# Kernel tuning notes

Measured on AMD Instinct MI355X. Metric: run time of the kernel, lower is better.

## Reference

```python
import jax, jax.numpy as jnp
import numpy as np
from jax import lax

B, T, L, D, K, VOCAB = 64, 128, 32, 128, 64, 50000


def setup_inputs() -> dict:
    key = jax.random.key(0)
    ks = jax.random.split(key, 8)
    prgrph = jax.random.randint(ks[0], (B, T, L), 0, VOCAB, dtype=jnp.int32)
    prgrph_mask = jax.random.randint(ks[1], (B, T, L), 0, 2, dtype=jnp.int32).astype(bool)
    embedding_matrix = jax.random.normal(ks[2], (VOCAB, D), dtype=jnp.float32)
    positional_mask = jax.random.normal(ks[3], (L, D), dtype=jnp.float32)
    Uw = jax.random.normal(ks[4], (D, D), dtype=jnp.float32) * 0.05
    Vw = jax.random.normal(ks[5], (D, D), dtype=jnp.float32) * 0.05
    Ww = jax.random.normal(ks[6], (D, D), dtype=jnp.float32) * 0.05
    keys = jax.random.normal(ks[7], (B, K, D), dtype=jnp.float32)
    return {"prgrph": prgrph, "prgrph_mask": prgrph_mask,
            "embedding_matrix": embedding_matrix, "positional_mask": positional_mask,
            "Uw": Uw, "Vw": Vw, "Ww": Ww, "keys": keys}


def _entity_scan(enc, sent_mask, keys, Uw, Vw, Ww):
    # enc: [B,T,D] encoded sentences; sent_mask: [B,T] bool; keys: [B,K,D]
    h0 = jnp.zeros_like(keys)  # initial entity hidden state = zeros

    def step(h, xs):
        s, m = xs  # s: [B,D], m: [B]
        # Eq 2: gate = sigmoid(s . h + s . k)  -> [B,K]
        g = jax.nn.sigmoid(jnp.einsum('bkd,bd->bk', h + keys, s))
        # Eq 3: h_tilda = sigmoid(h U + k V + s W)  -> [B,K,D]
        h_tilda = jax.nn.sigmoid(
            jnp.einsum('bkd,de->bke', h, Uw)
            + jnp.einsum('bkd,de->bke', keys, Vw)
            + (s @ Ww)[:, None, :])
        # Eq 4-5: add gated update, L2-normalize over embedding dim
        hn = h + g[..., None] * h_tilda
        hn = hn / jnp.sqrt(jnp.maximum(jnp.sum(hn * hn, axis=-1, keepdims=True), 1e-12))
        # only paragraphs with an active sentence at this step are updated
        h = jnp.where(m[:, None, None], hn, h)
        return h, None

    h_last, _ = lax.scan(step, h0, (jnp.swapaxes(enc, 0, 1), sent_mask.T))
    return h_last


def reference(prgrph, prgrph_mask, embedding_matrix, positional_mask, Uw, Vw, Ww, keys):
    # embed words; padded words contribute zero to the sentence encoding
    emb = embedding_matrix[prgrph] * prgrph_mask[..., None].astype(embedding_matrix.dtype)  # [B,T,L,D]
    # Sent_encoder: weighted bag of words with learned positional mask
    enc = jnp.einsum('btld,ld->btd', emb, positional_mask)  # [B,T,D]
    sent_mask = jnp.any(prgrph_mask, axis=2)  # [B,T]
    return _entity_scan(enc, sent_mask, keys, Uw, Vw, Ww)  # [B,K,D]
```

## Files before the change

### kernel.cpp

```cpp
#include <hip/hip_runtime.h>
#include <hip/hip_bf16.h>
#include <stdint.h>

#define B_ 64
#define T_ 128
#define L_ 32
#define D_ 128
#define K_ 64

#define FLAG_OFF 0
#define SM_OFF   256
#define ENC_OFF  (SM_OFF + B_*T_)
#define SW_OFF   (ENC_OFF + B_*T_*D_)
#define KS_OFF   (SW_OFF + B_*T_*D_)
#define KV_OFF   (KS_OFF + B_*T_*K_)

typedef __attribute__((ext_vector_type(8))) short short8b;
typedef __attribute__((ext_vector_type(4))) float f32x4;

__device__ __forceinline__ float sigmoidf_(float x){ return 1.0f/(1.0f + __expf(-x)); }

__device__ __forceinline__ unsigned short bfb(float x){
  __hip_bfloat16 h = __float2bfloat16(x);
  return __builtin_bit_cast(unsigned short, h);
}
__device__ __forceinline__ float bf2f(unsigned short u){
  return __uint_as_float(((unsigned)u) << 16);
}

__global__ __launch_bounds__(256) void k_detect(const uint8_t* __restrict__ m,
                                                int* __restrict__ flags){
  const unsigned* w = (const unsigned*)m;
  const int base = blockIdx.x * 512;
  unsigned acc = 0;
  acc |= w[base + threadIdx.x]       & 0xFFFFFF00u;
  acc |= w[base + threadIdx.x + 256] & 0xFFFFFF00u;
  int any = __syncthreads_or((int)(acc != 0u));
  if(threadIdx.x == 0) flags[blockIdx.x] = any;
}

__global__ __launch_bounds__(128) void k_enc(const int* __restrict__ prg,
                                             const uint8_t* __restrict__ pm8,
                                             const float* __restrict__ emb,
                                             const float* __restrict__ pos,
                                             const float* __restrict__ Ww,
                                             const float* __restrict__ keys,
                                             float* __restrict__ W){
  const int bt = blockIdx.x;
  const int b  = bt / T_;
  const int d  = threadIdx.x;
  int myf  = ((const int*)W)[FLAG_OFF + (d & 127)];
  int flag = __syncthreads_or(myf);
  __shared__ float keysl[K_*129];
  __shared__ float encl[D_];
  for(int r=0;r<K_;r++) keysl[r*129 + d] = keys[(b*K_ + r)*D_ + d];
  const int* pmi = (const int*)pm8;
  float acc = 0.f; int anym = 0;
  for(int l=0;l<L_;l++){
    int off = bt*L_ + l;
    int m = flag ? (int)pm8[off] : pmi[off];
    if(m){
      anym = 1;
      int idx = prg[off];
      acc += emb[idx*D_ + d] * pos[l*D_ + d];
    }
  }
  encl[d] = acc;
  W[ENC_OFF + bt*D_ + d] = acc;
  __syncthreads();
  float sw = 0.f;
  for(int e=0;e<D_;e++) sw += encl[e] * Ww[e*D_ + d];
  W[SW_OFF + bt*D_ + d] = sw;
  if(d < K_){
    float ks = 0.f;
    for(int dd=0;dd<D_;dd++) ks += keysl[d*129 + dd] * encl[dd];
    W[KS_OFF + bt*K_ + d] = ks;
  }
  if(d==0) W[SM_OFF + bt] = anym ? 1.f : 0.f;
}

__global__ __launch_bounds__(128) void k_kv(const float* __restrict__ keys,
                                            const float* __restrict__ Vw,
                                            float* __restrict__ W){
  const int bk = blockIdx.x;
  const int d  = threadIdx.x;
  __shared__ float kr[D_];
  kr[d] = keys[bk*D_ + d];
  __syncthreads();
  float acc = 0.f;
  for(int e=0;e<D_;e++) acc += kr[e] * Vw[e*D_ + d];
  W[KV_OFF + bk*D_ + d] = acc;
}

__global__ __launch_bounds__(64,1) void k_scan(const float* __restrict__ W,
                                               const float* __restrict__ Uw,
                                               float* __restrict__ out){
  const int b    = blockIdx.x >> 2;
  const int kg   = blockIdx.x & 3;
  const int lane = threadIdx.x;
  const int e    = lane & 15;
  const int q    = lane >> 4;
  const int swz  = (e << 2) & 0x3C;

  __shared__ unsigned hrep[2048];

  short8b ufrag[8][4];
  #pragma unroll
  for(int rt=0; rt<8; ++rt){
    #pragma unroll
    for(int kc=0; kc<4; ++kc){
      const float* src = &Uw[(32*kc + 8*q)*D_ + 16*rt + e];
      short8b f;
      #pragma unroll
      for(int j=0;j<8;++j) f[j] = (short)bfb(src[j*D_]);
      ufrag[rt][kc] = f;
    }
  }
  f32x4 kvv[8];
  {
    const float* kvp = &W[KV_OFF + (b*K_ + kg*16 + e)*D_ + 4*q];
    #pragma unroll
    for(int rt=0;rt<8;++rt) kvv[rt] = *(const f32x4*)&kvp[16*rt];
  }
  f32x4 hY[8];
  #pragma unroll
  for(int rt=0;rt<8;++rt) hY[rt] = 0.f;

  const float* ENC = &W[ENC_OFF + b*T_*D_];
  const float* SWg = &W[SW_OFF  + b*T_*D_];
  const float* KSg = &W[KS_OFF  + b*T_*K_];
  const float* SM  = &W[SM_OFF  + b*T_];

  auto loadstep = [&](int t, f32x4 (&sv)[8], f32x4 (&sw)[8], float& ks, float& sm){
    const float* sp = &ENC[t*D_ + 4*q];
    const float* wp = &SWg[t*D_ + 4*q];
    #pragma unroll
    for(int rt=0;rt<8;++rt){
      sv[rt] = *(const f32x4*)&sp[16*rt];
      sw[rt] = *(const f32x4*)&wp[16*rt];
    }
    ks = KSg[t*K_ + kg*16 + e];
    sm = SM[t];
  };

  auto dostep = [&](const f32x4 (&sv)[8], const f32x4 (&swv)[8], float ks, float sm){
    if(sm != 0.f){
      float gs = 0.f;
      #pragma unroll
      for(int rt=0;rt<8;++rt)
        gs += hY[rt][0]*sv[rt][0] + hY[rt][1]*sv[rt][1]
            + hY[rt][2]*sv[rt][2] + hY[rt][3]*sv[rt][3];
      gs += __shfl_xor(gs,16);
      gs += __shfl_xor(gs,32);
      float g = sigmoidf_(gs + ks);

      #pragma unroll
      for(int rt=0;rt<8;++rt){
        float x0=hY[rt][0], x1=hY[rt][1], x2=hY[rt][2], x3=hY[rt][3];
        unsigned short h0=bfb(x0), h1=bfb(x1), h2=bfb(x2), h3=bfb(x3);
        unsigned hi0 = ((unsigned)h1<<16) | h0;
        unsigned hi1 = ((unsigned)h3<<16) | h2;
        unsigned short l0=bfb(x0-bf2f(h0)), l1=bfb(x1-bf2f(h1));
        unsigned short l2=bfb(x2-bf2f(h2)), l3=bfb(x3-bf2f(h3));
        unsigned lo0 = ((unsigned)l1<<16) | l0;
        unsigned lo1 = ((unsigned)l3<<16) | l2;
        int a = e*64 + ((8*rt + 2*q) ^ swz);
        uint2 wh; wh.x=hi0; wh.y=hi1;
        uint2 wl; wl.x=lo0; wl.y=lo1;
        *(uint2*)&hrep[a]        = wh;
        *(uint2*)&hrep[1024 + a] = wl;
      }
      __syncthreads();
      short8b bhi[4], blo[4];
      #pragma unroll
      for(int kc=0;kc<4;++kc){
        int a = e*64 + ((16*kc + 4*q) ^ swz);
        bhi[kc] = *(const short8b*)&hrep[a];
        blo[kc] = *(const short8b*)&hrep[1024 + a];
      }
      __syncthreads();

      f32x4 acc[8];
      #pragma unroll
      for(int rt=0;rt<8;++rt) acc[rt] = kvv[rt];
      #pragma unroll
      for(int rt=0;rt<8;++rt){
        #pragma unroll
        for(int kc=0;kc<4;++kc){
          acc[rt] = __builtin_amdgcn_mfma_f32_16x16x32_bf16(ufrag[rt][kc], bhi[kc], acc[rt], 0,0,0);
          acc[rt] = __builtin_amdgcn_mfma_f32_16x16x32_bf16(ufrag[rt][kc], blo[kc], acc[rt], 0,0,0);
        }
      }

      f32x4 hn[8];
      float nrm = 0.f;
      #pragma unroll
      for(int rt=0;rt<8;++rt){
        #pragma unroll
        for(int r=0;r<4;++r){
          float x  = acc[rt][r] + swv[rt][r];
          float ht = sigmoidf_(x);
          float v  = hY[rt][r] + g*ht;
          hn[rt][r] = v;
          nrm += v*v;
        }
      }
      nrm += __shfl_xor(nrm,16);
      nrm += __shfl_xor(nrm,32);
      float rn = rsqrtf(fmaxf(nrm, 1e-12f));
      #pragma unroll
      for(int rt=0;rt<8;++rt){
        #pragma unroll
        for(int r=0;r<4;++r) hY[rt][r] = hn[rt][r]*rn;
      }
    }
  };

  f32x4 svA[8], swA[8], svB[8], swB[8];
  float ksA, smA, ksB, smB;
  loadstep(0, svA, swA, ksA, smA);
  #pragma unroll 1
  for(int t=0; t<T_; t+=2){
    loadstep(t+1, svB, swB, ksB, smB);
    dostep(svA, swA, ksA, smA);
    int t2 = (t+2 < T_) ? (t+2) : 0;
    loadstep(t2, svA, swA, ksA, smA);
    dostep(svB, swB, ksB, smB);
  }

  float* op = &out[(b*K_ + kg*16 + e)*D_ + 4*q];
  #pragma unroll
  for(int rt=0;rt<8;++rt) *(f32x4*)&op[16*rt] = hY[rt];
}

extern "C" void kernel_launch(void* const* d_in, const int* in_sizes, int n_in,
                              void* d_out, int out_size, void* d_ws, size_t ws_size,
                              hipStream_t stream) {
  const int*     prg  = (const int*)d_in[0];
  const uint8_t* pm   = (const uint8_t*)d_in[1];
  const float*   emb  = (const float*)d_in[2];
  const float*   pos  = (const float*)d_in[3];
  const float*   Uw   = (const float*)d_in[4];
  const float*   Vw   = (const float*)d_in[5];
  const float*   Ww   = (const float*)d_in[6];
  const float*   keys = (const float*)d_in[7];
  float* W   = (float*)d_ws;
  float* out = (float*)d_out;

  hipLaunchKernelGGL(k_detect, dim3(128),    dim3(256), 0, stream, pm, (int*)d_ws + FLAG_OFF);
  hipLaunchKernelGGL(k_enc,    dim3(B_*T_),  dim3(128), 0, stream, prg, pm, emb, pos, Ww, keys, W);
  hipLaunchKernelGGL(k_kv,     dim3(B_*K_),  dim3(128), 0, stream, keys, Vw, W);
  hipLaunchKernelGGL(k_scan,   dim3(B_*4),   dim3(64),  0, stream, W, Uw, out);
}
```

Before: 512.8 us.

## Defer L2 normalization in entity scan and drop intra-wave barriers

```diff
diff --git a/kernel.cpp b/kernel.cpp
--- a/kernel.cpp
+++ b/kernel.cpp
@@ -122,41 +122,34 @@
     #pragma unroll
     for(int rt=0;rt<8;++rt) kvv[rt] = *(const f32x4*)&kvp[16*rt];
   }
-  f32x4 hY[8];
-  #pragma unroll
-  for(int rt=0;rt<8;++rt) hY[rt] = 0.f;
+  f32x4 vY[8];
+  #pragma unroll
+  for(int rt=0;rt<8;++rt) vY[rt] = 0.f;
 
   const float* ENC = &W[ENC_OFF + b*T_*D_];
   const float* SWg = &W[SW_OFF  + b*T_*D_];
   const float* KSg = &W[KS_OFF  + b*T_*K_];
   const float* SM  = &W[SM_OFF  + b*T_];
 
-  auto loadstep = [&](int t, f32x4 (&sv)[8], f32x4 (&sw)[8], float& ks, float& sm){
+  auto loadstep = [&](int t, f32x4 (&sv)[8], f32x4 (&sk)[8], float& ks, float& sm){
     const float* sp = &ENC[t*D_ + 4*q];
     const float* wp = &SWg[t*D_ + 4*q];
     #pragma unroll
     for(int rt=0;rt<8;++rt){
       sv[rt] = *(const f32x4*)&sp[16*rt];
-      sw[rt] = *(const f32x4*)&wp[16*rt];
+      f32x4 w = *(const f32x4*)&wp[16*rt];
+      #pragma unroll
+      for(int r=0;r<4;++r) sk[rt][r] = w[r] + kvv[rt][r];
     }
     ks = KSg[t*K_ + kg*16 + e];
     sm = SM[t];
   };
 
-  auto dostep = [&](const f32x4 (&sv)[8], const f32x4 (&swv)[8], float ks, float sm){
+  auto dostep = [&](const f32x4 (&sv)[8], const f32x4 (&skv)[8], float ks, float sm){
     if(sm != 0.f){
-      float gs = 0.f;
-      #pragma unroll
-      for(int rt=0;rt<8;++rt)
-        gs += hY[rt][0]*sv[rt][0] + hY[rt][1]*sv[rt][1]
-            + hY[rt][2]*sv[rt][2] + hY[rt][3]*sv[rt][3];
-      gs += __shfl_xor(gs,16);
-      gs += __shfl_xor(gs,32);
-      float g = sigmoidf_(gs + ks);
-
-      #pragma unroll
-      for(int rt=0;rt<8;++rt){
-        float x0=hY[rt][0], x1=hY[rt][1], x2=hY[rt][2], x3=hY[rt][3];
+      #pragma unroll
+      for(int rt=0;rt<8;++rt){
+        float x0=vY[rt][0], x1=vY[rt][1], x2=vY[rt][2], x3=vY[rt][3];
         unsigned short h0=bfb(x0), h1=bfb(x1), h2=bfb(x2), h3=bfb(x3);
         unsigned hi0 = ((unsigned)h1<<16) | h0;
         unsigned hi1 = ((unsigned)h3<<16) | h2;
@@ -170,7 +163,22 @@
         *(uint2*)&hrep[a]        = wh;
         *(uint2*)&hrep[1024 + a] = wl;
       }
-      __syncthreads();
+      float ns = 0.f, gs = 0.f;
+      #pragma unroll
+      for(int rt=0;rt<8;++rt){
+        #pragma unroll
+        for(int r=0;r<4;++r){
+          ns += vY[rt][r]*vY[rt][r];
+          gs += vY[rt][r]*sv[rt][r];
+        }
+      }
+      ns += __shfl_xor(ns,16);
+      ns += __shfl_xor(ns,32);
+      gs += __shfl_xor(gs,16);
+      gs += __shfl_xor(gs,32);
+      float n = rsqrtf(fmaxf(ns, 1e-12f));
+      float g = sigmoidf_(fmaf(n, gs, ks));
+
       short8b bhi[4], blo[4];
       #pragma unroll
       for(int kc=0;kc<4;++kc){
@@ -178,11 +186,10 @@
         bhi[kc] = *(const short8b*)&hrep[a];
         blo[kc] = *(const short8b*)&hrep[1024 + a];
       }
-      __syncthreads();
 
       f32x4 acc[8];
       #pragma unroll
-      for(int rt=0;rt<8;++rt) acc[rt] = kvv[rt];
+      for(int rt=0;rt<8;++rt) acc[rt] = 0.f;
       #pragma unroll
       for(int rt=0;rt<8;++rt){
         #pragma unroll
@@ -192,45 +199,47 @@
         }
       }
 
-      f32x4 hn[8];
-      float nrm = 0.f;
       #pragma unroll
       for(int rt=0;rt<8;++rt){
         #pragma unroll
         for(int r=0;r<4;++r){
-          float x  = acc[rt][r] + swv[rt][r];
+          float x  = fmaf(n, acc[rt][r], skv[rt][r]);
           float ht = sigmoidf_(x);
-          float v  = hY[rt][r] + g*ht;
-          hn[rt][r] = v;
-          nrm += v*v;
+          vY[rt][r] = fmaf(g, ht, n*vY[rt][r]);
         }
       }
-      nrm += __shfl_xor(nrm,16);
-      nrm += __shfl_xor(nrm,32);
-      float rn = rsqrtf(fmaxf(nrm, 1e-12f));
-      #pragma unroll
-      for(int rt=0;rt<8;++rt){
-        #pragma unroll
-        for(int r=0;r<4;++r) hY[rt][r] = hn[rt][r]*rn;
-      }
     }
   };
 
-  f32x4 svA[8], swA[8], svB[8], swB[8];
+  f32x4 svA[8], skA[8], svB[8], skB[8];
   float ksA, smA, ksB, smB;
-  loadstep(0, svA, swA, ksA, smA);
+  loadstep(0, svA, skA, ksA, smA);
   #pragma unroll 1
   for(int t=0; t<T_; t+=2){
-    loadstep(t+1, svB, swB, ksB, smB);
-    dostep(svA, swA, ksA, smA);
+    loadstep(t+1, svB, skB, ksB, smB);
+    dostep(svA, skA, ksA, smA);
     int t2 = (t+2 < T_) ? (t+2) : 0;
-    loadstep(t2, svA, swA, ksA, smA);
-    dostep(svB, swB, ksB, smB);
-  }
-
+    loadstep(t2, svA, skA, ksA, smA);
+    dostep(svB, skB, ksB, smB);
+  }
+
+  float ns = 0.f;
+  #pragma unroll
+  for(int rt=0;rt<8;++rt){
+    #pragma unroll
+    for(int r=0;r<4;++r) ns += vY[rt][r]*vY[rt][r];
+  }
+  ns += __shfl_xor(ns,16);
+  ns += __shfl_xor(ns,32);
+  float n = rsqrtf(fmaxf(ns, 1e-12f));
   float* op = &out[(b*K_ + kg*16 + e)*D_ + 4*q];
   #pragma unroll
-  for(int rt=0;rt<8;++rt) *(f32x4*)&op[16*rt] = hY[rt];
+  for(int rt=0;rt<8;++rt){
+    f32x4 o;
+    #pragma unroll
+    for(int r=0;r<4;++r) o[r] = vY[rt][r]*n;
+    *(f32x4*)&op[16*rt] = o;
+  }
 }
 
 extern "C" void kernel_launch(void* const* d_in, const int* in_sizes, int n_in,
```

Result: slower. 554.8 us (+8.2%).
